# Performance work log

Hardware: AMD Instinct MI355X
Metric: run time of the kernel (lower is better)

The kernel has to match this reference:

```python
import jax, jax.numpy as jnp
import numpy as np

T, E, DIM, HID = 8192, 8, 1024, 2048


def setup_inputs() -> dict:
    key = jax.random.key(0)
    k1, k2, k3 = jax.random.split(key, 3)
    x = jax.random.normal(k1, (T, DIM), dtype=jnp.float32)
    w1 = jax.random.normal(k2, (E, HID, DIM), dtype=jnp.float32)
    w2 = jax.random.normal(k3, (E, DIM, HID), dtype=jnp.float32)
    # Tokens are pre-grouped by expert; counts must sum exactly to T.
    num_tokens_per_expert = jnp.full((E,), T // E, dtype=jnp.int32)
    return {"x": x, "w1": w1, "w2": w2, "num_tokens_per_expert": num_tokens_per_expert}


def reference(x, w1, w2, num_tokens_per_expert):
    # Faithful to torch._grouped_mm path: bf16 casts, two ragged grouped GEMMs,
    # result cast back to x.dtype.
    gs = num_tokens_per_expert.astype(jnp.int32)
    xb = x.astype(jnp.bfloat16)                                  # [T, dim]
    w1t = jnp.swapaxes(w1.astype(jnp.bfloat16), -2, -1)          # [E, dim, hid]
    w2t = jnp.swapaxes(w2.astype(jnp.bfloat16), -2, -1)          # [E, hid, dim]
    h = jax.lax.ragged_dot(xb, w1t, gs)                          # [T, hid] bf16
    out = jax.lax.ragged_dot(h, w2t, gs)                         # [T, dim] bf16
    return out.astype(x.dtype)
```

## Files before the change

kernel.cpp:

```cpp
#include <hip/hip_runtime.h>
#include <stdint.h>

#define T_TOK 8192
#define NEXP  8
#define DIMSZ 1024
#define HIDSZ 2048

typedef __attribute__((ext_vector_type(4))) float f32x4;
typedef __attribute__((ext_vector_type(8))) short s16x8;


__device__ __forceinline__ uint16_t f2bf(float f) {
  uint32_t u = __builtin_bit_cast(uint32_t, f);
  u += 0x7fffu + ((u >> 16) & 1u);
  return (uint16_t)(u >> 16);
}

__device__ __forceinline__ uint32_t pkbf(float a, float b) {
  return (uint32_t)f2bf(a) | ((uint32_t)f2bf(b) << 16);
}

__device__ __forceinline__ void gload_lds16(const uint16_t* g, const uint16_t* lds_base) {
  __builtin_amdgcn_global_load_lds(
      (const __attribute__((address_space(1))) uint32_t*)(uintptr_t)g,
      (__attribute__((address_space(3))) uint32_t*)(uint32_t)(uintptr_t)lds_base,
      16, 0, 0);
}


__global__ void cvt_x(const float* __restrict__ x, uint16_t* __restrict__ xb,
                      const int* __restrict__ counts, int* __restrict__ offs,
                      int* __restrict__ toffs) {
  if (blockIdx.x == 0 && threadIdx.x == 0) {
    int s = 0, ts = 0;
    for (int e = 0; e < NEXP; ++e) {
      offs[e] = s; toffs[e] = ts;
      s += counts[e]; ts += (counts[e] + 127) >> 7;
    }
    offs[NEXP] = s; toffs[NEXP] = ts;
  }
  const size_t i = blockIdx.x * (size_t)blockDim.x + threadIdx.x;
  const float4* p = (const float4*)x + 4 * i;
  float4 a = p[0], b = p[1], c = p[2], d = p[3];
  uint4 o0, o1;
  o0.x = pkbf(a.x, a.y); o0.y = pkbf(a.z, a.w);
  o0.z = pkbf(b.x, b.y); o0.w = pkbf(b.z, b.w);
  o1.x = pkbf(c.x, c.y); o1.y = pkbf(c.z, c.w);
  o1.z = pkbf(d.x, d.y); o1.w = pkbf(d.z, d.w);
  uint4* q = (uint4*)xb + 2 * i;
  q[0] = o0;
  q[1] = o1;
}

template <bool OUT_BF16>
__global__ __launch_bounds__(256, 3)
void gemm_grouped(const uint16_t* __restrict__ A, const float* __restrict__ B,
                  void* __restrict__ C, const int* __restrict__ offs,
                  const int* __restrict__ toffs, int N, int K, int lognt) {
  __shared__ __align__(16) uint16_t As[128 * 64];
  __shared__ __align__(16) uint16_t Bs[128 * 64];

  const int mtg = blockIdx.x >> lognt;
  const int nt  = blockIdx.x & ((1 << lognt) - 1);
  if (mtg >= toffs[NEXP]) return;
  int e = 0;
#pragma unroll
  for (int i = 1; i < NEXP; ++i) e += (toffs[i] <= mtg) ? 1 : 0;
  const int mt      = mtg - toffs[e];
  const int m_start = offs[e];
  const int m_count = offs[e + 1] - m_start;
  const int m0      = mt * 128;
  int valid_m = m_count - m0;
  if (valid_m > 128) valid_m = 128;
  const int n0 = nt * 128;

  const int tid  = threadIdx.x;
  const int w    = tid >> 6;
  const int lane = tid & 63;
  const int wm = w & 1, wn = w >> 1;

  const uint16_t* gA = A + (size_t)m_start * K;
  const float*    gB = B + (size_t)e * N * K;

  const uint16_t* ap[4];
#pragma unroll
  for (int c = 0; c < 4; ++c) {
    const int r  = w * 32 + c * 8 + (lane >> 3);
    const int q8 = ((lane & 7) ^ ((r >> 1) & 7)) * 8;
    const int ra = (r < valid_m) ? r : (valid_m - 1);
    ap[c] = gA + (size_t)(m0 + ra) * K + q8;
  }

  const float* bp[4];
  int bwoff[4];
#pragma unroll
  for (int c = 0; c < 4; ++c) {
    const int r = w * 32 + c * 8 + (lane >> 3);
    bp[c] = gB + (size_t)(n0 + r) * K + (lane & 7) * 8;
    bwoff[c] = r * 64 + (((lane & 7) ^ ((r >> 1) & 7)) * 8);
  }

  const int fr = lane & 15;
  const int f0 = ((lane >> 4) ^ ((fr >> 1) & 7)) * 8;

  f32x4 acc[4][4];
#pragma unroll
  for (int mi = 0; mi < 4; ++mi)
#pragma unroll
    for (int ni = 0; ni < 4; ++ni) acc[mi][ni] = (f32x4){0.f, 0.f, 0.f, 0.f};

  float4 bq[8];
#pragma unroll
  for (int c = 0; c < 4; ++c) {
    bq[2 * c]     = *(const float4*)bp[c];
    bq[2 * c + 1] = *(const float4*)(bp[c] + 4);
    bp[c] += 64;
  }

  for (int k0 = 0; k0 < K; k0 += 64) {
    __syncthreads();
#pragma unroll
    for (int c = 0; c < 4; ++c) {
      gload_lds16(ap[c], &As[(w * 32 + c * 8) * 64]);
      ap[c] += 64;
    }
#pragma unroll
    for (int c = 0; c < 4; ++c) {
      uint4 o;
      o.x = pkbf(bq[2 * c].x,     bq[2 * c].y);
      o.y = pkbf(bq[2 * c].z,     bq[2 * c].w);
      o.z = pkbf(bq[2 * c + 1].x, bq[2 * c + 1].y);
      o.w = pkbf(bq[2 * c + 1].z, bq[2 * c + 1].w);
      *(uint4*)&Bs[bwoff[c]] = o;
    }
    __syncthreads();

    if (k0 + 64 < K) {
#pragma unroll
      for (int c = 0; c < 4; ++c) {
        bq[2 * c]     = *(const float4*)bp[c];
        bq[2 * c + 1] = *(const float4*)(bp[c] + 4);
        bp[c] += 64;
      }
    }
    asm volatile("" ::: "memory");

#pragma unroll
    for (int kk = 0; kk < 2; ++kk) {
      const int fk = f0 ^ (kk << 5);
      s16x8 af[4], bf[4];
#pragma unroll
      for (int mi = 0; mi < 4; ++mi)
        af[mi] = *(const s16x8*)&As[(wm * 64 + mi * 16 + fr) * 64 + fk];
#pragma unroll
      for (int ni = 0; ni < 4; ++ni)
        bf[ni] = *(const s16x8*)&Bs[(wn * 64 + ni * 16 + fr) * 64 + fk];
#pragma unroll
      for (int mi = 0; mi < 4; ++mi)
#pragma unroll
        for (int ni = 0; ni < 4; ++ni)
          acc[mi][ni] = __builtin_amdgcn_mfma_f32_16x16x32_bf16(af[mi], bf[ni], acc[mi][ni], 0, 0, 0);
    }
  }

  const int cq = (lane >> 4) * 4;
  const int cc = lane & 15;
#pragma unroll
  for (int mi = 0; mi < 4; ++mi) {
#pragma unroll
    for (int r = 0; r < 4; ++r) {
      const int rt = wm * 64 + mi * 16 + cq + r;
      if (rt < valid_m) {
        const size_t rowoff = (size_t)(m_start + m0 + rt) * N;
#pragma unroll
        for (int ni = 0; ni < 4; ++ni) {
          const int col = n0 + wn * 64 + ni * 16 + cc;
          const float v = acc[mi][ni][r];
          if (OUT_BF16) {
            ((uint16_t*)C)[rowoff + col] = f2bf(v);
          } else {
            const uint32_t b = (uint32_t)f2bf(v) << 16;
            ((float*)C)[rowoff + col] = __builtin_bit_cast(float, b);
          }
        }
      }
    }
  }
}


extern "C" void kernel_launch(void* const* d_in, const int* in_sizes, int n_in,
                              void* d_out, int out_size, void* d_ws, size_t ws_size,
                              hipStream_t stream) {
  const float* x  = (const float*)d_in[0];
  const float* w1 = (const float*)d_in[1];
  const float* w2 = (const float*)d_in[2];
  const int* cnt  = (const int*)d_in[3];
  float* out = (float*)d_out;

  char* ws = (char*)d_ws;
  uint16_t* xb = (uint16_t*)(ws);
  uint16_t* h  = (uint16_t*)(ws + 16777216);
  int* offs    = (int*)(ws + 50331648);
  int* toffs   = offs + 9;

  cvt_x<<<2048, 256, 0, stream>>>(x, xb, cnt, offs, toffs);

  const int MAX_MT = T_TOK / 128 + NEXP - 1;

  gemm_grouped<true><<<MAX_MT * 16, 256, 0, stream>>>(
      xb, w1, (void*)h, offs, toffs, HIDSZ, DIMSZ, 4);

  gemm_grouped<false><<<MAX_MT * 8, 256, 0, stream>>>(
      h, w2, (void*)out, offs, toffs, DIMSZ, HIDSZ, 3);
}
```

Measured before the change: 287.8 us.

## Double-buffer LDS tiles in grouped GEMM and remap blocks across XCDs

Makes the A/B shared-memory tiles double-buffered so the next K-tile's global loads (async A into LDS, B into registers) are issued before the MFMA work on the current tile, leaving one barrier per iteration instead of two. It also remaps block IDs so that consecutive logical tiles land on the same XCD, which should improve L2 reuse of weights and activations. Doubling LDS use to 64KB per block means launch bounds drop from 3 to 2 blocks per CU, which costs occupancy.

```diff
diff --git a/kernel.cpp b/kernel.cpp
--- a/kernel.cpp
+++ b/kernel.cpp
@@ -53,15 +53,20 @@
 }
 
 template <bool OUT_BF16>
-__global__ __launch_bounds__(256, 3)
+__global__ __launch_bounds__(256, 2)
 void gemm_grouped(const uint16_t* __restrict__ A, const float* __restrict__ B,
                   void* __restrict__ C, const int* __restrict__ offs,
                   const int* __restrict__ toffs, int N, int K, int lognt) {
-  __shared__ __align__(16) uint16_t As[128 * 64];
-  __shared__ __align__(16) uint16_t Bs[128 * 64];
-
-  const int mtg = blockIdx.x >> lognt;
-  const int nt  = blockIdx.x & ((1 << lognt) - 1);
+  __shared__ __align__(16) uint16_t As[2][128 * 64];
+  __shared__ __align__(16) uint16_t Bs[2][128 * 64];
+
+  const int nwg  = gridDim.x;
+  const int orig = blockIdx.x;
+  const int qc = nwg >> 3, rc = nwg & 7, xcd = orig & 7;
+  const int bid = (xcd < rc ? xcd * (qc + 1) : rc * (qc + 1) + (xcd - rc) * qc) + (orig >> 3);
+
+  const int mtg = bid >> lognt;
+  const int nt  = bid & ((1 << lognt) - 1);
   if (mtg >= toffs[NEXP]) return;
   int e = 0;
 #pragma unroll
@@ -110,57 +115,81 @@
     for (int ni = 0; ni < 4; ++ni) acc[mi][ni] = (f32x4){0.f, 0.f, 0.f, 0.f};
 
   float4 bq[8];
+  const int NT = K >> 6;
+
 #pragma unroll
   for (int c = 0; c < 4; ++c) {
     bq[2 * c]     = *(const float4*)bp[c];
     bq[2 * c + 1] = *(const float4*)(bp[c] + 4);
     bp[c] += 64;
   }
-
-  for (int k0 = 0; k0 < K; k0 += 64) {
-    __syncthreads();
-#pragma unroll
-    for (int c = 0; c < 4; ++c) {
-      gload_lds16(ap[c], &As[(w * 32 + c * 8) * 64]);
-      ap[c] += 64;
-    }
-#pragma unroll
-    for (int c = 0; c < 4; ++c) {
-      uint4 o;
-      o.x = pkbf(bq[2 * c].x,     bq[2 * c].y);
-      o.y = pkbf(bq[2 * c].z,     bq[2 * c].w);
-      o.z = pkbf(bq[2 * c + 1].x, bq[2 * c + 1].y);
-      o.w = pkbf(bq[2 * c + 1].z, bq[2 * c + 1].w);
-      *(uint4*)&Bs[bwoff[c]] = o;
-    }
-    __syncthreads();
-
-    if (k0 + 64 < K) {
+#pragma unroll
+  for (int c = 0; c < 4; ++c) {
+    gload_lds16(ap[c], &As[0][(w * 32 + c * 8) * 64]);
+    ap[c] += 64;
+  }
+#pragma unroll
+  for (int c = 0; c < 4; ++c) {
+    uint4 o;
+    o.x = pkbf(bq[2 * c].x,     bq[2 * c].y);
+    o.y = pkbf(bq[2 * c].z,     bq[2 * c].w);
+    o.z = pkbf(bq[2 * c + 1].x, bq[2 * c + 1].y);
+    o.w = pkbf(bq[2 * c + 1].z, bq[2 * c + 1].w);
+    *(uint4*)&Bs[0][bwoff[c]] = o;
+  }
+  __syncthreads();
+
+  int cur = 0;
+  for (int t = 0; t < NT; ++t) {
+    const int nxt = cur ^ 1;
+    const bool more = (t + 1 < NT);
+
+    if (more) {
 #pragma unroll
       for (int c = 0; c < 4; ++c) {
         bq[2 * c]     = *(const float4*)bp[c];
         bq[2 * c + 1] = *(const float4*)(bp[c] + 4);
         bp[c] += 64;
       }
-    }
-    asm volatile("" ::: "memory");
-
+#pragma unroll
+      for (int c = 0; c < 4; ++c) {
+        gload_lds16(ap[c], &As[nxt][(w * 32 + c * 8) * 64]);
+        ap[c] += 64;
+      }
+    }
+
+    const uint16_t* curA = As[cur];
+    const uint16_t* curB = Bs[cur];
 #pragma unroll
     for (int kk = 0; kk < 2; ++kk) {
       const int fk = f0 ^ (kk << 5);
       s16x8 af[4], bf[4];
 #pragma unroll
       for (int mi = 0; mi < 4; ++mi)
-        af[mi] = *(const s16x8*)&As[(wm * 64 + mi * 16 + fr) * 64 + fk];
+        af[mi] = *(const s16x8*)&curA[(wm * 64 + mi * 16 + fr) * 64 + fk];
 #pragma unroll
       for (int ni = 0; ni < 4; ++ni)
-        bf[ni] = *(const s16x8*)&Bs[(wn * 64 + ni * 16 + fr) * 64 + fk];
+        bf[ni] = *(const s16x8*)&curB[(wn * 64 + ni * 16 + fr) * 64 + fk];
 #pragma unroll
       for (int mi = 0; mi < 4; ++mi)
 #pragma unroll
         for (int ni = 0; ni < 4; ++ni)
           acc[mi][ni] = __builtin_amdgcn_mfma_f32_16x16x32_bf16(af[mi], bf[ni], acc[mi][ni], 0, 0, 0);
     }
+
+    if (more) {
+#pragma unroll
+      for (int c = 0; c < 4; ++c) {
+        uint4 o;
+        o.x = pkbf(bq[2 * c].x,     bq[2 * c].y);
+        o.y = pkbf(bq[2 * c].z,     bq[2 * c].w);
+        o.z = pkbf(bq[2 * c + 1].x, bq[2 * c + 1].y);
+        o.w = pkbf(bq[2 * c + 1].z, bq[2 * c + 1].w);
+        *(uint4*)&Bs[nxt][bwoff[c]] = o;
+      }
+    }
+    __syncthreads();
+    cur = nxt;
   }
 
   const int cq = (lane >> 4) * 4;
```

After: 356.3 us. 23.8% more time.

## Double-buffer A tile in LDS and remap block IDs across XCDs

Applied to the files above, without the earlier changes.

Adds a second LDS buffer for the A tile so the asynchronous global-to-LDS load for the next K step is issued before the MFMA work on the current step, overlapping load latency with compute. B stays single-buffered, with a barrier pair around its fp32-to-bf16 store after compute. Block indices are also remapped so consecutive logical tiles land on the same XCD, which is meant to improve L2 reuse. The extra LDS per block may reduce occupancy below the launch-bounds target.

```diff
diff --git a/kernel.cpp b/kernel.cpp
--- a/kernel.cpp
+++ b/kernel.cpp
@@ -57,11 +57,17 @@
 void gemm_grouped(const uint16_t* __restrict__ A, const float* __restrict__ B,
                   void* __restrict__ C, const int* __restrict__ offs,
                   const int* __restrict__ toffs, int N, int K, int lognt) {
-  __shared__ __align__(16) uint16_t As[128 * 64];
+  __shared__ __align__(16) uint16_t As0[128 * 64];
+  __shared__ __align__(16) uint16_t As1[128 * 64];
   __shared__ __align__(16) uint16_t Bs[128 * 64];
 
-  const int mtg = blockIdx.x >> lognt;
-  const int nt  = blockIdx.x & ((1 << lognt) - 1);
+  const int nwg  = gridDim.x;
+  const int orig = blockIdx.x;
+  const int qc = nwg >> 3, rc = nwg & 7, xcd = orig & 7;
+  const int bid = (xcd < rc ? xcd * (qc + 1) : rc * (qc + 1) + (xcd - rc) * qc) + (orig >> 3);
+
+  const int mtg = bid >> lognt;
+  const int nt  = bid & ((1 << lognt) - 1);
   if (mtg >= toffs[NEXP]) return;
   int e = 0;
 #pragma unroll
@@ -110,58 +116,83 @@
     for (int ni = 0; ni < 4; ++ni) acc[mi][ni] = (f32x4){0.f, 0.f, 0.f, 0.f};
 
   float4 bq[8];
+  const int NT = K >> 6;
+
 #pragma unroll
   for (int c = 0; c < 4; ++c) {
     bq[2 * c]     = *(const float4*)bp[c];
     bq[2 * c + 1] = *(const float4*)(bp[c] + 4);
     bp[c] += 64;
   }
-
-  for (int k0 = 0; k0 < K; k0 += 64) {
-    __syncthreads();
-#pragma unroll
-    for (int c = 0; c < 4; ++c) {
-      gload_lds16(ap[c], &As[(w * 32 + c * 8) * 64]);
-      ap[c] += 64;
-    }
-#pragma unroll
-    for (int c = 0; c < 4; ++c) {
-      uint4 o;
-      o.x = pkbf(bq[2 * c].x,     bq[2 * c].y);
-      o.y = pkbf(bq[2 * c].z,     bq[2 * c].w);
-      o.z = pkbf(bq[2 * c + 1].x, bq[2 * c + 1].y);
-      o.w = pkbf(bq[2 * c + 1].z, bq[2 * c + 1].w);
-      *(uint4*)&Bs[bwoff[c]] = o;
-    }
-    __syncthreads();
-
-    if (k0 + 64 < K) {
-#pragma unroll
-      for (int c = 0; c < 4; ++c) {
-        bq[2 * c]     = *(const float4*)bp[c];
-        bq[2 * c + 1] = *(const float4*)(bp[c] + 4);
-        bp[c] += 64;
-      }
-    }
-    asm volatile("" ::: "memory");
-
-#pragma unroll
-    for (int kk = 0; kk < 2; ++kk) {
-      const int fk = f0 ^ (kk << 5);
-      s16x8 af[4], bf[4];
-#pragma unroll
-      for (int mi = 0; mi < 4; ++mi)
-        af[mi] = *(const s16x8*)&As[(wm * 64 + mi * 16 + fr) * 64 + fk];
-#pragma unroll
-      for (int ni = 0; ni < 4; ++ni)
-        bf[ni] = *(const s16x8*)&Bs[(wn * 64 + ni * 16 + fr) * 64 + fk];
-#pragma unroll
-      for (int mi = 0; mi < 4; ++mi)
-#pragma unroll
-        for (int ni = 0; ni < 4; ++ni)
-          acc[mi][ni] = __builtin_amdgcn_mfma_f32_16x16x32_bf16(af[mi], bf[ni], acc[mi][ni], 0, 0, 0);
-    }
-  }
+#pragma unroll
+  for (int c = 0; c < 4; ++c) {
+    gload_lds16(ap[c], &As0[(w * 32 + c * 8) * 64]);
+    ap[c] += 64;
+  }
+#pragma unroll
+  for (int c = 0; c < 4; ++c) {
+    uint4 o;
+    o.x = pkbf(bq[2 * c].x,     bq[2 * c].y);
+    o.y = pkbf(bq[2 * c].z,     bq[2 * c].w);
+    o.z = pkbf(bq[2 * c + 1].x, bq[2 * c + 1].y);
+    o.w = pkbf(bq[2 * c + 1].z, bq[2 * c + 1].w);
+    *(uint4*)&Bs[bwoff[c]] = o;
+  }
+  __syncthreads();
+
+#define STEP(AR, AW, T)                                                         \
+  {                                                                             \
+    const bool more = ((T) + 1 < NT);                                           \
+    if (more) {                                                                 \
+      _Pragma("unroll")                                                         \
+      for (int c = 0; c < 4; ++c) {                                             \
+        bq[2 * c]     = *(const float4*)bp[c];                                  \
+        bq[2 * c + 1] = *(const float4*)(bp[c] + 4);                            \
+        bp[c] += 64;                                                            \
+      }                                                                         \
+      _Pragma("unroll")                                                         \
+      for (int c = 0; c < 4; ++c) {                                             \
+        gload_lds16(ap[c], &AW[(w * 32 + c * 8) * 64]);                         \
+        ap[c] += 64;                                                            \
+      }                                                                         \
+    }                                                                           \
+    _Pragma("unroll")                                                           \
+    for (int kk = 0; kk < 2; ++kk) {                                            \
+      const int fk = f0 ^ (kk << 5);                                            \
+      s16x8 af[4], bf[4];                                                       \
+      _Pragma("unroll")                                                         \
+      for (int mi = 0; mi < 4; ++mi)                                            \
+        af[mi] = *(const s16x8*)&AR[(wm * 64 + mi * 16 + fr) * 64 + fk];        \
+      _Pragma("unroll")                                                         \
+      for (int ni = 0; ni < 4; ++ni)                                            \
+        bf[ni] = *(const s16x8*)&Bs[(wn * 64 + ni * 16 + fr) * 64 + fk];        \
+      _Pragma("unroll")                                                         \
+      for (int mi = 0; mi < 4; ++mi)                                            \
+        _Pragma("unroll")                                                       \
+        for (int ni = 0; ni < 4; ++ni)                                          \
+          acc[mi][ni] = __builtin_amdgcn_mfma_f32_16x16x32_bf16(                \
+              af[mi], bf[ni], acc[mi][ni], 0, 0, 0);                            \
+    }                                                                           \
+    if (more) {                                                                 \
+      __syncthreads();       \
+      _Pragma("unroll")                                                         \
+      for (int c = 0; c < 4; ++c) {                                             \
+        uint4 o;                                                                \
+        o.x = pkbf(bq[2 * c].x,     bq[2 * c].y);                               \
+        o.y = pkbf(bq[2 * c].z,     bq[2 * c].w);                               \
+        o.z = pkbf(bq[2 * c + 1].x, bq[2 * c + 1].y);                           \
+        o.w = pkbf(bq[2 * c + 1].z, bq[2 * c + 1].w);                           \
+        *(uint4*)&Bs[bwoff[c]] = o;                                             \
+      }                                                                         \
+      __syncthreads();                 \
+    }                                                                           \
+  }
+
+  for (int t = 0; t < NT; t += 2) {
+    STEP(As0, As1, t);
+    STEP(As1, As0, t + 1);
+  }
+#undef STEP
 
   const int cq = (lane >> 4) * 4;
   const int cc = lane & 15;
```

Result: slower. 704.2 us (+144.7%).
